# Performance work log

Measured on AMD Instinct MI355X. Metric: run time of the kernel, lower is better.

## Reference

```python
import jax, jax.numpy as jnp
import numpy as np

NUM_SAMPLES = 10
MIN_DIST_PTS = 8
TOP_K = 10
GRID_SIZE = 4
GAP = 0.1


def sample_line_points(seg):
    # seg: [N,2,2] (endpoints, ij coords). Vectorized version of the per-group linspace loop.
    lengths = jnp.linalg.norm(seg[:, 0] - seg[:, 1], axis=1)
    n_samp = jnp.clip(jnp.floor(lengths / MIN_DIST_PTS), 2, NUM_SAMPLES)  # [N]
    t = jnp.arange(NUM_SAMPLES, dtype=seg.dtype)  # [S]
    interval = (seg[:, 1] - seg[:, 0]) / (n_samp[:, None] - 1)  # [N,2]
    pts = seg[:, None, 0, :] + t[None, :, None] * interval[:, None, :]  # [N,S,2]
    valid = t[None, :] < n_samp[:, None]  # [N,S]
    pts = jnp.where(valid[..., None], pts, 0.0)  # original zero-pads invalid samples
    return pts, valid


def grid_sample_norm(desc, pts, img_size):
    # desc: [D,Hc,Wc]; pts: [P,2] (i,j) pixel coords in image of size img_size=(H,W).
    # Replicates kornia normalize_pixel_coordinates + F.grid_sample(align_corners=False,
    # bilinear, zero padding), then L2-normalize along D.
    D, Hc, Wc = desc.shape
    H, W = img_size
    gx = 2.0 * pts[:, 1] / (W - 1) - 1.0
    gy = 2.0 * pts[:, 0] / (H - 1) - 1.0
    ix = ((gx + 1.0) * Wc - 1.0) / 2.0
    iy = ((gy + 1.0) * Hc - 1.0) / 2.0
    x0 = jnp.floor(ix)
    y0 = jnp.floor(iy)
    wx1 = ix - x0
    wy1 = iy - y0
    x0i = x0.astype(jnp.int32)
    y0i = y0.astype(jnp.int32)

    def gather(yi, xi):
        inb = (xi >= 0) & (xi < Wc) & (yi >= 0) & (yi < Hc)
        v = desc[:, jnp.clip(yi, 0, Hc - 1), jnp.clip(xi, 0, Wc - 1)]  # [D,P]
        return v * inb

    v = (gather(y0i, x0i) * (1 - wy1) * (1 - wx1)
         + gather(y0i, x0i + 1) * (1 - wy1) * wx1
         + gather(y0i + 1, x0i) * wy1 * (1 - wx1)
         + gather(y0i + 1, x0i + 1) * wy1 * wx1)
    nrm = jnp.linalg.norm(v, axis=0, keepdims=True)
    return v / jnp.maximum(nrm, 1e-12)


def needleman_wunsch(scores):
    # scores: [B,n,m]. Row-wise scan; the within-row dependency
    # v[j+1]=max(v[j], max(prev[j+1], prev[j]+s)) is a prefix-max (cummax).
    b, n, m = scores.shape
    s = scores - GAP
    init = jnp.zeros((b, m + 1), s.dtype)

    def step(prev, row):  # prev [B,m+1], row [B,m]
        a = jnp.maximum(prev[:, 1:], prev[:, :-1] + row)
        new = jnp.maximum(jax.lax.cummax(a, axis=1), 0.0)
        return jnp.concatenate([jnp.zeros((b, 1), s.dtype), new], axis=1), None

    final, _ = jax.lax.scan(step, init, jnp.swapaxes(s, 0, 1))
    return final[:, -1]


def nw_candidate_scores(scores):
    # scores: [N1,N2,S,S] -> (nw [N1,2k], topk [N1,k])
    ls1 = jnp.max(scores, axis=3)
    v1 = ls1 != -1
    ls1 = jnp.where(v1, ls1, 0.0).sum(2) / v1.sum(2)
    ls2 = jnp.max(scores, axis=2)
    v2 = ls2 != -1
    ls2 = jnp.where(v2, ls2, 0.0).sum(2) / v2.sum(2)
    line_scores = (ls1 + ls2) / 2
    topk = jnp.argsort(line_scores, axis=1)[:, -TOP_K:]  # [N1,k]
    top_scores = jnp.take_along_axis(scores, topk[:, :, None, None], axis=1)  # [N1,k,S,S]
    top_scores = jnp.concatenate([top_scores, jnp.flip(top_scores, axis=-1)], axis=1)  # [N1,2k,S,S]
    N1, t2k, n, m = top_scores.shape
    nw = needleman_wunsch(top_scores.reshape(N1 * t2k, n, m)).reshape(N1, t2k)
    return nw, topk


def filter_and_match(scores):
    nw, topk = nw_candidate_scores(scores)
    t2k = nw.shape[1]
    best = jnp.argmax(nw, axis=1) % (t2k // 2)
    return jnp.take_along_axis(topk, best[:, None], axis=1)[:, 0]


def compute_scores(line_seg1, line_seg2, desc1, desc2):
    S = NUM_SAMPLES
    img1 = (desc1.shape[2] * GRID_SIZE, desc1.shape[3] * GRID_SIZE)
    img2 = (desc2.shape[2] * GRID_SIZE, desc2.shape[3] * GRID_SIZE)
    pts1, val1 = sample_line_points(line_seg1)
    pts2, val2 = sample_line_points(line_seg2)
    d1 = grid_sample_norm(desc1[0], pts1.reshape(-1, 2), img1)  # [D, N1*S]
    d2 = grid_sample_norm(desc2[0], pts2.reshape(-1, 2), img2)  # [D, N2*S]
    sc = d1.T @ d2  # [N1*S, N2*S]
    sc = jnp.where(val1.reshape(-1)[:, None], sc, -1.0)
    sc = jnp.where(val2.reshape(-1)[None, :], sc, -1.0)
    N1, N2 = line_seg1.shape[0], line_seg2.shape[0]
    return sc.reshape(N1, S, N2, S).transpose(0, 2, 1, 3)  # [N1,N2,S,S]


def reference(line_seg1, line_seg2, desc1, desc2):
    scores = compute_scores(line_seg1, line_seg2, desc1, desc2)
    matches = filter_and_match(scores)
    # cross check
    matches2 = filter_and_match(scores.transpose(1, 0, 3, 2))
    mutual = matches2[matches] == jnp.arange(line_seg1.shape[0])
    return jnp.where(mutual, matches, -1).astype(jnp.int32)


def setup_inputs() -> dict:
    key = jax.random.key(0)
    k1, k2, k3, k4 = jax.random.split(key, 4)
    IMG = 512.0
    line_seg1 = jax.random.uniform(k1, (512, 2, 2), dtype=jnp.float32) * (IMG - 1.0)
    line_seg2 = jax.random.uniform(k2, (512, 2, 2), dtype=jnp.float32) * (IMG - 1.0)
    desc1 = jax.random.normal(k3, (1, 128, 128, 128), dtype=jnp.float32)
    desc2 = jax.random.normal(k4, (1, 128, 128, 128), dtype=jnp.float32)
    return {"line_seg1": line_seg1, "line_seg2": line_seg2, "desc1": desc1, "desc2": desc2}
```

## Files before the change

### kernel.cpp

```cpp
#include <hip/hip_runtime.h>
#include <cmath>

#define NL 512
#define SS 10
#define DD 128
#define HWC (128 * 128)

typedef _Float16 f16x8 __attribute__((ext_vector_type(8)));
typedef float f32x4 __attribute__((ext_vector_type(4)));

__device__ __forceinline__ void gload_lds16(const void* g, void* l)
{
    __builtin_amdgcn_global_load_lds(
        (__attribute__((address_space(1))) void*)const_cast<void*>(g),
        (__attribute__((address_space(3))) void*)l, 16, 0, 0);
}

__global__ __launch_bounds__(256) void transpose_kernel(
    const float* __restrict__ in1, const float* __restrict__ in2,
    float* __restrict__ out1, float* __restrict__ out2)
{
    const float* in = blockIdx.z ? in2 : in1;
    float* out = blockIdx.z ? out2 : out1;
    __shared__ float tile[32][33];
    int hw0 = blockIdx.x * 32;
    int d0 = blockIdx.y * 32;
    int tx = threadIdx.x, ty = threadIdx.y;
#pragma unroll
    for (int j = 0; j < 32; j += 8)
        tile[ty + j][tx] = in[(size_t)(d0 + ty + j) * HWC + hw0 + tx];
    __syncthreads();
#pragma unroll
    for (int j = 0; j < 32; j += 8)
        out[(size_t)(hw0 + ty + j) * DD + d0 + tx] = tile[tx][ty + j];
}

__device__ __forceinline__ float fetchd(const float* __restrict__ dt, int y, int x, int d)
{
    bool inb = (x >= 0) && (x < 128) && (y >= 0) && (y < 128);
    int yc = y < 0 ? 0 : (y > 127 ? 127 : y);
    int xc = x < 0 ? 0 : (x > 127 ? 127 : x);
    float v = dt[((size_t)(yc * 128 + xc)) * DD + d];
    return inb ? v : 0.0f;
}

__global__ __launch_bounds__(640) void sample_kernel(
    const float* __restrict__ seg1, const float* __restrict__ seg2,
    const float* __restrict__ dt1, const float* __restrict__ dt2,
    float* __restrict__ dd1, float* __restrict__ dd2,
    _Float16* __restrict__ h1, _Float16* __restrict__ m1,
    _Float16* __restrict__ h2, _Float16* __restrict__ m2,
    int* __restrict__ v1, int* __restrict__ v2)
{
#pragma clang fp contract(off)
    int L = blockIdx.x;
    int img = blockIdx.y;
    const float* seg = img ? seg2 : seg1;
    const float* dt = img ? dt2 : dt1;
    float* dd = img ? dd2 : dd1;
    _Float16* ph = img ? h2 : h1;
    _Float16* pm = img ? m2 : m1;
    int* vv = img ? v2 : v1;

    float p0y = seg[L * 4 + 0], p0x = seg[L * 4 + 1];
    float p1y = seg[L * 4 + 2], p1x = seg[L * 4 + 3];
    float dy = p0y - p1y, dx = p0x - p1x;
    float len = sqrtf(dy * dy + dx * dx);
    float nf = floorf(len / 8.0f);
    nf = fminf(fmaxf(nf, 2.0f), 10.0f);
    int ni = (int)nf;
    float ivy = (p1y - p0y) / (nf - 1.0f);
    float ivx = (p1x - p0x) / (nf - 1.0f);

    int t = threadIdx.x >> 6;
    int lane = threadIdx.x & 63;
    int pt = L * SS + t;
    bool val = t < ni;
    int d0 = lane, d1 = lane + 64;
    float o0 = 0.0f, o1 = 0.0f;
    if (val) {
        float py = p0y + (float)t * ivy;
        float px = p0x + (float)t * ivx;
        float gx = 2.0f * px / 511.0f - 1.0f;
        float gy = 2.0f * py / 511.0f - 1.0f;
        float ix = ((gx + 1.0f) * 128.0f - 1.0f) / 2.0f;
        float iy = ((gy + 1.0f) * 128.0f - 1.0f) / 2.0f;
        float x0f = floorf(ix), y0f = floorf(iy);
        float wx = ix - x0f, wy = iy - y0f;
        int x0 = (int)x0f, y0 = (int)y0f;
        float a00 = fetchd(dt, y0, x0, d0),         b00 = fetchd(dt, y0, x0, d1);
        float a01 = fetchd(dt, y0, x0 + 1, d0),     b01 = fetchd(dt, y0, x0 + 1, d1);
        float a10 = fetchd(dt, y0 + 1, x0, d0),     b10 = fetchd(dt, y0 + 1, x0, d1);
        float a11 = fetchd(dt, y0 + 1, x0 + 1, d0), b11 = fetchd(dt, y0 + 1, x0 + 1, d1);
        float omwx = 1.0f - wx, omwy = 1.0f - wy;
        float va = a00 * omwy * omwx + a01 * omwy * wx + a10 * wy * omwx + a11 * wy * wx;
        float vb = b00 * omwy * omwx + b01 * omwy * wx + b10 * wy * omwx + b11 * wy * wx;
        float s = va * va + vb * vb;
#pragma unroll
        for (int m = 1; m < 64; m <<= 1) s += __shfl_xor(s, m);
        float nrm = sqrtf(s);
        o0 = va / fmaxf(nrm, 1e-12f);
        o1 = vb / fmaxf(nrm, 1e-12f);
    }
    dd[(size_t)pt * DD + d0] = o0;
    dd[(size_t)pt * DD + d1] = o1;
    float xs0 = o0 * 256.0f;
    _Float16 hh0 = (_Float16)xs0;
    _Float16 mm0 = (_Float16)(xs0 - (float)hh0);
    float xs1 = o1 * 256.0f;
    _Float16 hh1 = (_Float16)xs1;
    _Float16 mm1 = (_Float16)(xs1 - (float)hh1);
    int po0 = ((pt >> 4) << 11) + ((d0 >> 3) << 7) + ((pt & 15) << 3) + (d0 & 7);
    int po1 = ((pt >> 4) << 11) + ((d1 >> 3) << 7) + ((pt & 15) << 3) + (d1 & 7);
    ph[po0] = hh0; pm[po0] = mm0;
    ph[po1] = hh1; pm[po1] = mm1;
    if (lane == 0) vv[pt] = val ? 1 : 0;
}

__device__ __forceinline__ void stage_ks(
    const _Float16* __restrict__ ah, const _Float16* __restrict__ am,
    const _Float16* __restrict__ bh, const _Float16* __restrict__ bm,
    int bi, int bj, int ks, int wave, int lane, char* dst)
{
#pragma unroll
    for (int c = 0; c < 8; ++c) {
        int chunk = wave + (c << 3);
        if (chunk < 60) {
            int side = chunk >= 20;
            int rem = side ? chunk - 20 : chunk;
            int nb = side ? 20 : 10;
            int plane = rem >= nb;
            int pb = plane ? rem - nb : rem;
            const _Float16* base = side ? (plane ? bm : bh) : (plane ? am : ah);
            int gpb = side ? (bj * 20 + pb) : (bi * 10 + pb);
            size_t off = ((size_t)gpb << 11) + (ks << 9) + (lane << 3);
            gload_lds16(base + off, dst + (chunk << 10));
        }
    }
}

__global__ __launch_bounds__(512, 2) void gemm_ls_kernel(
    const _Float16* __restrict__ ah_, const _Float16* __restrict__ am_,
    const _Float16* __restrict__ bh_, const _Float16* __restrict__ bm_,
    const int* __restrict__ v1, const int* __restrict__ v2,
    float* __restrict__ ls, float* __restrict__ lsT)
{
    __shared__ __align__(16) char smem[122880];
    int tid = threadIdx.x;
    int wave = tid >> 6, lane = tid & 63;
    int wr = wave >> 2, wc = wave & 3;

    int flat = blockIdx.x;
    int xcd = flat & 7, n = flat >> 3;
    int bi = (xcd >> 1) * 8 + (n >> 3);
    int bj = (xcd & 1) * 8 + (n & 7);

    int fro = ((lane >> 4) << 8) + ((lane & 15) << 4);

    f32x4 zz = {0.0f, 0.0f, 0.0f, 0.0f};
    f32x4 acc[5][5];
#pragma unroll
    for (int i = 0; i < 5; ++i)
#pragma unroll
        for (int j = 0; j < 5; ++j) acc[i][j] = zz;

    stage_ks(ah_, am_, bh_, bm_, bi, bj, 0, wave, lane, smem);

#pragma unroll 1
    for (int ks = 0; ks < 4; ++ks) {
        char* buf = smem + ((ks & 1) ? 61440 : 0);
        if (ks < 3) {
            stage_ks(ah_, am_, bh_, bm_, bi, bj, ks + 1, wave, lane,
                     smem + (((ks + 1) & 1) ? 61440 : 0));
            if (wave < 4) asm volatile("s_waitcnt vmcnt(8)" ::: "memory");
            else          asm volatile("s_waitcnt vmcnt(7)" ::: "memory");
        } else {
            asm volatile("s_waitcnt vmcnt(0)" ::: "memory");
        }
        __builtin_amdgcn_sched_barrier(0);
        __builtin_amdgcn_s_barrier();
        __builtin_amdgcn_sched_barrier(0);

        f16x8 B0[5], B1[5];
#pragma unroll
        for (int j = 0; j < 5; ++j) {
            int pb = wc * 5 + j;
            B0[j] = *(const f16x8*)(buf + ((20 + pb) << 10) + fro);
            B1[j] = *(const f16x8*)(buf + ((40 + pb) << 10) + fro);
        }
#pragma unroll
        for (int i = 0; i < 5; ++i) {
            int pb = wr * 5 + i;
            f16x8 fh = *(const f16x8*)(buf + (pb << 10) + fro);
            f16x8 fm = *(const f16x8*)(buf + ((10 + pb) << 10) + fro);
#pragma unroll
            for (int j = 0; j < 5; ++j) {
                f32x4 t = acc[i][j];
                t = __builtin_amdgcn_mfma_f32_16x16x32_f16(fh, B0[j], t, 0, 0, 0);
                t = __builtin_amdgcn_mfma_f32_16x16x32_f16(fh, B1[j], t, 0, 0, 0);
                t = __builtin_amdgcn_mfma_f32_16x16x32_f16(fm, B0[j], t, 0, 0, 0);
                acc[i][j] = t;
            }
        }
        __builtin_amdgcn_sched_barrier(0);
        __builtin_amdgcn_s_barrier();
        __builtin_amdgcn_sched_barrier(0);
    }

    float* scr = (float*)smem;
    const float rescale = 1.0f / 65536.0f;
    for (int half = 0; half < 2; ++half) {
        __syncthreads();
        if (wr == half) {
            float* reg = scr + wc * 6464;
#pragma unroll
            for (int i = 0; i < 5; ++i)
#pragma unroll
                for (int j = 0; j < 5; ++j)
#pragma unroll
                    for (int r = 0; r < 4; ++r) {
                        int row = i * 16 + ((lane >> 4) << 2) + r;
                        int col = j * 16 + (lane & 15);
                        int pi = row / 10, s = row - pi * 10;
                        int pj = col / 10, t = col - pj * 10;
                        reg[(pi * 8 + pj) * 101 + s * 10 + t] = acc[i][j][r] * rescale;
                    }
            asm volatile("s_waitcnt lgkmcnt(0)" ::: "memory");
            const float* mp = reg + lane * 101;
            int iL = bi * 16 + half * 8 + (lane >> 3);
            int jL = bj * 32 + wc * 8 + (lane & 7);
            int va[10], vb[10];
#pragma unroll
            for (int s = 0; s < 10; ++s) va[s] = v1[iL * 10 + s];
#pragma unroll
            for (int t = 0; t < 10; ++t) vb[t] = v2[jL * 10 + t];
            float cmx[10];
#pragma unroll
            for (int t = 0; t < 10; ++t) cmx[t] = -3.0e38f;
            float sum1 = 0.0f; int c1 = 0;
#pragma unroll
            for (int s = 0; s < 10; ++s) {
                float rmx = -3.0e38f;
#pragma unroll
                for (int t = 0; t < 10; ++t) {
                    float v = (va[s] && vb[t]) ? mp[s * 10 + t] : -1.0f;
                    rmx = fmaxf(rmx, v);
                    cmx[t] = fmaxf(cmx[t], v);
                }
                if (rmx != -1.0f) { sum1 += rmx; c1++; }
            }
            float sum2 = 0.0f; int c2 = 0;
#pragma unroll
            for (int t = 0; t < 10; ++t) {
                if (cmx[t] != -1.0f) { sum2 += cmx[t]; c2++; }
            }
            float out = (sum1 / (float)c1 + sum2 / (float)c2) * 0.5f;
            ls[(size_t)iL * NL + jL] = out;
            lsT[(size_t)jL * NL + iL] = out;
        }
    }
}

__global__ __launch_bounds__(256) void nw_kernel(
    const float* __restrict__ d1, const float* __restrict__ d2,
    const int* __restrict__ v1, const int* __restrict__ v2,
    const float* __restrict__ ls, const float* __restrict__ lsT,
    int* __restrict__ topkg, float* __restrict__ nwout)
{
    int L = blockIdx.x;
    int dir = blockIdx.y;
    const float* Ad = dir ? d2 : d1;
    const float* Bd = dir ? d1 : d2;
    const int* vA = dir ? v2 : v1;
    const int* vB = dir ? v1 : v2;
    const float* src = dir ? &lsT[(size_t)L * NL] : &ls[(size_t)L * NL];

    __shared__ float Asl[10 * 132];
    __shared__ float Bsl[10][1320];
    __shared__ float M[10][110];
    __shared__ int vam[10], tks[10];

    int tid = threadIdx.x;
    if (tid < 10) vam[tid] = vA[L * 10 + tid];
#pragma unroll
    for (int it = 0; it < 5; ++it) {
        int idx = tid + it * 256;
        int row = idx >> 7, col = idx & 127;
        Asl[row * 132 + col] = Ad[((size_t)L * 10 + row) * DD + col];
    }
    if (tid < 64) {
        int lane = tid;
        float v[8];
#pragma unroll
        for (int it = 0; it < 8; ++it) v[it] = src[it * 64 + lane];
        for (int p = 9; p >= 0; --p) {
            float bv = -3.0e38f;
            int bi_ = -1;
#pragma unroll
            for (int it = 0; it < 8; ++it) {
                int j = it * 64 + lane;
                bool better = (v[it] > bv) || (v[it] == bv && j > bi_);
                if (better) { bv = v[it]; bi_ = j; }
            }
#pragma unroll
            for (int m = 1; m < 64; m <<= 1) {
                float ov = __shfl_xor(bv, m);
                int oi = __shfl_xor(bi_, m);
                bool better = (ov > bv) || (ov == bv && oi > bi_);
                if (better) { bv = ov; bi_ = oi; }
            }
            if ((bi_ & 63) == lane) v[bi_ >> 6] = -3.0e38f;
            if (lane == 0) tks[p] = bi_;
        }
    }
    __syncthreads();
    if (tid < 10) topkg[(size_t)(dir * NL + L) * 10 + tid] = tks[tid];
#pragma unroll
    for (int it = 0; it < 50; ++it) {
        int idx = tid + it * 256;
        int c = idx / 1280;
        int rem = idx - c * 1280;
        int row = rem >> 7, col = rem & 127;
        Bsl[c][row * 132 + col] = Bd[((size_t)tks[c] * 10 + row) * DD + col];
    }
    __syncthreads();
#pragma unroll
    for (int it = 0; it < 4; ++it) {
        int w = tid + it * 256;
        if (w < 1000) {
            int c = w / 100;
            int rem = w - c * 100;
            int s = rem / 10, t = rem - s * 10;
            const float4* ap = (const float4*)&Asl[s * 132];
            const float4* bp = (const float4*)&Bsl[c][t * 132];
            float acc = 0.0f;
#pragma unroll
            for (int k = 0; k < 32; ++k) {
                float4 a = ap[k], b = bp[k];
                acc = fmaf(a.x, b.x, acc);
                acc = fmaf(a.y, b.y, acc);
                acc = fmaf(a.z, b.z, acc);
                acc = fmaf(a.w, b.w, acc);
            }
            int ok = vam[s] && vB[tks[c] * 10 + t];
            M[c][s * 11 + t] = ok ? acc : -1.0f;
        }
    }
    __syncthreads();

    if (tid < 20) {
        int c = tid % 10, f = tid / 10;
        float prev[11];
#pragma unroll
        for (int p = 0; p < 11; ++p) prev[p] = 0.0f;
#pragma unroll
        for (int s = 0; s < 10; ++s) {
            float oldp = prev[0];
            float run = -3.0e38f;
#pragma unroll
            for (int t = 0; t < 10; ++t) {
                int tt = f ? (9 - t) : t;
                float sc = M[c][s * 11 + tt] - 0.1f;
                float pt1 = prev[t + 1];
                float av = fmaxf(pt1, oldp + sc);
                run = fmaxf(run, av);
                prev[t + 1] = fmaxf(run, 0.0f);
                oldp = pt1;
            }
        }
        nwout[((size_t)(dir * NL + L)) * 20 + f * 10 + c] = prev[10];
    }
}

__global__ __launch_bounds__(512) void final_kernel(
    const float* __restrict__ nw, const int* __restrict__ topk, int* __restrict__ out)
{
    __shared__ int m1[NL], m2[NL];
    int t = threadIdx.x;
    {
        const float* p = nw + (size_t)t * 20;
        float bb = -3.0e38f; int kk = 0;
        for (int k = 0; k < 20; ++k) {
            float v = p[k];
            if (v > bb) { bb = v; kk = k; }
        }
        m1[t] = topk[(size_t)t * 10 + (kk % 10)];
    }
    {
        const float* p = nw + (size_t)(NL + t) * 20;
        float bb = -3.0e38f; int kk = 0;
        for (int k = 0; k < 20; ++k) {
            float v = p[k];
            if (v > bb) { bb = v; kk = k; }
        }
        m2[t] = topk[(size_t)(NL + t) * 10 + (kk % 10)];
    }
    __syncthreads();
    int mt = m1[t];
    out[t] = (m2[mt] == t) ? mt : -1;
}

extern "C" void kernel_launch(void* const* d_in, const int* in_sizes, int n_in,
                              void* d_out, int out_size, void* d_ws, size_t ws_size,
                              hipStream_t stream)
{
    const float* seg1 = (const float*)d_in[0];
    const float* seg2 = (const float*)d_in[1];
    const float* desc1 = (const float*)d_in[2];
    const float* desc2 = (const float*)d_in[3];
    int* out = (int*)d_out;

    char* ws = (char*)d_ws;
    size_t off = 0;
    float* dt1 = (float*)(ws + off); off += (size_t)DD * HWC * 4;
    float* dt2 = (float*)(ws + off); off += (size_t)DD * HWC * 4;
    float* dd1 = (float*)(ws + off); off += (size_t)NL * SS * DD * 4;
    float* dd2 = (float*)(ws + off); off += (size_t)NL * SS * DD * 4;
    int* v1 = (int*)(ws + off); off += (size_t)NL * SS * 4;
    int* v2 = (int*)(ws + off); off += (size_t)NL * SS * 4;
    float* ls = (float*)(ws + off); off += (size_t)NL * NL * 4;
    float* lsT = (float*)(ws + off); off += (size_t)NL * NL * 4;
    int* topk = (int*)(ws + off); off += (size_t)2 * NL * 10 * 4;
    float* nwv = (float*)(ws + off); off += (size_t)2 * NL * 20 * 4;
    size_t PL = (size_t)NL * SS * DD;
    _Float16* h1 = (_Float16*)(ws + off); off += PL * 2;
    _Float16* m1 = (_Float16*)(ws + off); off += PL * 2;
    _Float16* h2 = (_Float16*)(ws + off); off += PL * 2;
    _Float16* m2 = (_Float16*)(ws + off); off += PL * 2;

    transpose_kernel<<<dim3(HWC / 32, DD / 32, 2), dim3(32, 8), 0, stream>>>(
        desc1, desc2, dt1, dt2);
    sample_kernel<<<dim3(NL, 2), 640, 0, stream>>>(
        seg1, seg2, dt1, dt2, dd1, dd2, h1, m1, h2, m2, v1, v2);
    gemm_ls_kernel<<<512, 512, 0, stream>>>(
        h1, m1, h2, m2, v1, v2, ls, lsT);
    nw_kernel<<<dim3(NL, 2), 256, 0, stream>>>(
        dd1, dd2, v1, v2, ls, lsT, topk, nwv);
    final_kernel<<<1, 512, 0, stream>>>(nwv, topk, out);
}
```

Measured before the change: 182.2 us.

## Replace descriptor transpose with per-channel LDS bilinear sampling plus normalize pass

Removes the full 16MB transpose of both descriptor maps. Each block now loads one 128x128 channel plane into shared memory and bilinearly samples every point from it, writing a channel-major raw buffer. A second kernel transposes tiles of that buffer, L2-normalizes each point and emits the fp32 and hi/lo fp16 split outputs. The aim is to avoid the large transpose read and write traffic, at the cost of an extra intermediate buffer, an extra launch, and a 64KB LDS footprint per block that limits occupancy.

```diff
diff --git a/kernel.cpp b/kernel.cpp
--- a/kernel.cpp
+++ b/kernel.cpp
@@ -5,6 +5,7 @@
 #define SS 10
 #define DD 128
 #define HWC (128 * 128)
+#define NPT (NL * SS)
 
 typedef _Float16 f16x8 __attribute__((ext_vector_type(8)));
 typedef float f32x4 __attribute__((ext_vector_type(4)));
@@ -16,105 +17,135 @@
         (__attribute__((address_space(3))) void*)l, 16, 0, 0);
 }
 
-__global__ __launch_bounds__(256) void transpose_kernel(
-    const float* __restrict__ in1, const float* __restrict__ in2,
-    float* __restrict__ out1, float* __restrict__ out2)
-{
-    const float* in = blockIdx.z ? in2 : in1;
-    float* out = blockIdx.z ? out2 : out1;
-    __shared__ float tile[32][33];
-    int hw0 = blockIdx.x * 32;
-    int d0 = blockIdx.y * 32;
-    int tx = threadIdx.x, ty = threadIdx.y;
-#pragma unroll
-    for (int j = 0; j < 32; j += 8)
-        tile[ty + j][tx] = in[(size_t)(d0 + ty + j) * HWC + hw0 + tx];
-    __syncthreads();
-#pragma unroll
-    for (int j = 0; j < 32; j += 8)
-        out[(size_t)(hw0 + ty + j) * DD + d0 + tx] = tile[tx][ty + j];
-}
-
-__device__ __forceinline__ float fetchd(const float* __restrict__ dt, int y, int x, int d)
-{
-    bool inb = (x >= 0) && (x < 128) && (y >= 0) && (y < 128);
-    int yc = y < 0 ? 0 : (y > 127 ? 127 : y);
-    int xc = x < 0 ? 0 : (x > 127 ? 127 : x);
-    float v = dt[((size_t)(yc * 128 + xc)) * DD + d];
-    return inb ? v : 0.0f;
-}
-
-__global__ __launch_bounds__(640) void sample_kernel(
-    const float* __restrict__ seg1, const float* __restrict__ seg2,
-    const float* __restrict__ dt1, const float* __restrict__ dt2,
-    float* __restrict__ dd1, float* __restrict__ dd2,
-    _Float16* __restrict__ h1, _Float16* __restrict__ m1,
-    _Float16* __restrict__ h2, _Float16* __restrict__ m2,
-    int* __restrict__ v1, int* __restrict__ v2)
+__device__ __forceinline__ void line_geom(const float* __restrict__ seg, int L,
+    float& p0y, float& p0x, float& ivy, float& ivx, int& ni)
 {
 #pragma clang fp contract(off)
-    int L = blockIdx.x;
-    int img = blockIdx.y;
-    const float* seg = img ? seg2 : seg1;
-    const float* dt = img ? dt2 : dt1;
-    float* dd = img ? dd2 : dd1;
-    _Float16* ph = img ? h2 : h1;
-    _Float16* pm = img ? m2 : m1;
-    int* vv = img ? v2 : v1;
-
-    float p0y = seg[L * 4 + 0], p0x = seg[L * 4 + 1];
+    p0y = seg[L * 4 + 0]; p0x = seg[L * 4 + 1];
     float p1y = seg[L * 4 + 2], p1x = seg[L * 4 + 3];
     float dy = p0y - p1y, dx = p0x - p1x;
     float len = sqrtf(dy * dy + dx * dx);
     float nf = floorf(len / 8.0f);
     nf = fminf(fmaxf(nf, 2.0f), 10.0f);
-    int ni = (int)nf;
-    float ivy = (p1y - p0y) / (nf - 1.0f);
-    float ivx = (p1x - p0x) / (nf - 1.0f);
-
-    int t = threadIdx.x >> 6;
-    int lane = threadIdx.x & 63;
-    int pt = L * SS + t;
-    bool val = t < ni;
-    int d0 = lane, d1 = lane + 64;
-    float o0 = 0.0f, o1 = 0.0f;
-    if (val) {
-        float py = p0y + (float)t * ivy;
-        float px = p0x + (float)t * ivx;
-        float gx = 2.0f * px / 511.0f - 1.0f;
-        float gy = 2.0f * py / 511.0f - 1.0f;
-        float ix = ((gx + 1.0f) * 128.0f - 1.0f) / 2.0f;
-        float iy = ((gy + 1.0f) * 128.0f - 1.0f) / 2.0f;
-        float x0f = floorf(ix), y0f = floorf(iy);
-        float wx = ix - x0f, wy = iy - y0f;
-        int x0 = (int)x0f, y0 = (int)y0f;
-        float a00 = fetchd(dt, y0, x0, d0),         b00 = fetchd(dt, y0, x0, d1);
-        float a01 = fetchd(dt, y0, x0 + 1, d0),     b01 = fetchd(dt, y0, x0 + 1, d1);
-        float a10 = fetchd(dt, y0 + 1, x0, d0),     b10 = fetchd(dt, y0 + 1, x0, d1);
-        float a11 = fetchd(dt, y0 + 1, x0 + 1, d0), b11 = fetchd(dt, y0 + 1, x0 + 1, d1);
-        float omwx = 1.0f - wx, omwy = 1.0f - wy;
-        float va = a00 * omwy * omwx + a01 * omwy * wx + a10 * wy * omwx + a11 * wy * wx;
-        float vb = b00 * omwy * omwx + b01 * omwy * wx + b10 * wy * omwx + b11 * wy * wx;
-        float s = va * va + vb * vb;
-#pragma unroll
-        for (int m = 1; m < 64; m <<= 1) s += __shfl_xor(s, m);
-        float nrm = sqrtf(s);
-        o0 = va / fmaxf(nrm, 1e-12f);
-        o1 = vb / fmaxf(nrm, 1e-12f);
-    }
-    dd[(size_t)pt * DD + d0] = o0;
-    dd[(size_t)pt * DD + d1] = o1;
-    float xs0 = o0 * 256.0f;
-    _Float16 hh0 = (_Float16)xs0;
-    _Float16 mm0 = (_Float16)(xs0 - (float)hh0);
-    float xs1 = o1 * 256.0f;
-    _Float16 hh1 = (_Float16)xs1;
-    _Float16 mm1 = (_Float16)(xs1 - (float)hh1);
-    int po0 = ((pt >> 4) << 11) + ((d0 >> 3) << 7) + ((pt & 15) << 3) + (d0 & 7);
-    int po1 = ((pt >> 4) << 11) + ((d1 >> 3) << 7) + ((pt & 15) << 3) + (d1 & 7);
-    ph[po0] = hh0; pm[po0] = mm0;
-    ph[po1] = hh1; pm[po1] = mm1;
-    if (lane == 0) vv[pt] = val ? 1 : 0;
+    ni = (int)nf;
+    ivy = (p1y - p0y) / (nf - 1.0f);
+    ivx = (p1x - p0x) / (nf - 1.0f);
+}
+
+__global__ __launch_bounds__(256) void bilin_kernel(
+    const float* __restrict__ seg1, const float* __restrict__ seg2,
+    const float* __restrict__ desc1, const float* __restrict__ desc2,
+    float* __restrict__ rawT1, float* __restrict__ rawT2)
+{
+#pragma clang fp contract(off)
+    int d = blockIdx.x;
+    int img = blockIdx.y;
+    const float* seg = img ? seg2 : seg1;
+    const float* desc = (img ? desc2 : desc1) + (size_t)d * HWC;
+    float* rawT = (img ? rawT2 : rawT1) + (size_t)d * NPT;
+
+    __shared__ float pd[HWC];
+    int tid = threadIdx.x;
+    const float4* src4 = (const float4*)desc;
+    float4* pd4 = (float4*)pd;
+#pragma unroll
+    for (int i = 0; i < 16; ++i) pd4[tid + i * 256] = src4[tid + i * 256];
+    __syncthreads();
+
+#pragma unroll
+    for (int i = 0; i < 20; ++i) {
+        int pt = tid + i * 256;
+        int L = pt / 10, t = pt - L * 10;
+        float p0y, p0x, ivy, ivx; int ni;
+        line_geom(seg, L, p0y, p0x, ivy, ivx, ni);
+        float outv = 0.0f;
+        if (t < ni) {
+            float py = p0y + (float)t * ivy;
+            float px = p0x + (float)t * ivx;
+            float gx = 2.0f * px / 511.0f - 1.0f;
+            float gy = 2.0f * py / 511.0f - 1.0f;
+            float ix = ((gx + 1.0f) * 128.0f - 1.0f) / 2.0f;
+            float iy = ((gy + 1.0f) * 128.0f - 1.0f) / 2.0f;
+            float x0f = floorf(ix), y0f = floorf(iy);
+            float wx = ix - x0f, wy = iy - y0f;
+            int x0 = (int)x0f, y0 = (int)y0f;
+            int xc0 = x0 < 0 ? 0 : (x0 > 127 ? 127 : x0);
+            int xc1 = (x0 + 1) < 0 ? 0 : ((x0 + 1) > 127 ? 127 : (x0 + 1));
+            int yc0 = y0 < 0 ? 0 : (y0 > 127 ? 127 : y0);
+            int yc1 = (y0 + 1) < 0 ? 0 : ((y0 + 1) > 127 ? 127 : (y0 + 1));
+            bool ibx0 = (x0 >= 0) && (x0 < 128), ibx1 = (x0 + 1 >= 0) && (x0 + 1 < 128);
+            bool iby0 = (y0 >= 0) && (y0 < 128), iby1 = (y0 + 1 >= 0) && (y0 + 1 < 128);
+            float g00 = (ibx0 && iby0) ? pd[yc0 * 128 + xc0] : 0.0f;
+            float g01 = (ibx1 && iby0) ? pd[yc0 * 128 + xc1] : 0.0f;
+            float g10 = (ibx0 && iby1) ? pd[yc1 * 128 + xc0] : 0.0f;
+            float g11 = (ibx1 && iby1) ? pd[yc1 * 128 + xc1] : 0.0f;
+            float omwx = 1.0f - wx, omwy = 1.0f - wy;
+            outv = g00 * omwy * omwx + g01 * omwy * wx + g10 * wy * omwx + g11 * wy * wx;
+        }
+        rawT[pt] = outv;
+    }
+}
+
+__global__ __launch_bounds__(256) void norm_split_kernel(
+    const float* __restrict__ seg1, const float* __restrict__ seg2,
+    const float* __restrict__ rawT1, const float* __restrict__ rawT2,
+    float* __restrict__ dd1, float* __restrict__ dd2,
+    _Float16* __restrict__ h1, _Float16* __restrict__ m1,
+    _Float16* __restrict__ h2, _Float16* __restrict__ m2,
+    int* __restrict__ v1, int* __restrict__ v2)
+{
+#pragma clang fp contract(off)
+    int img = blockIdx.y;
+    int p0 = blockIdx.x * 128;
+    const float* seg = img ? seg2 : seg1;
+    const float* rawT = img ? rawT2 : rawT1;
+    float* dd = img ? dd2 : dd1;
+    _Float16* ph = img ? h2 : h1;
+    _Float16* pm = img ? m2 : m1;
+    int* vv = img ? v2 : v1;
+
+    __shared__ float tile[128][129];
+    __shared__ float nr[128];
+    int tid = threadIdx.x;
+#pragma unroll
+    for (int i = 0; i < 16; ++i) {
+        int idx = tid + i * 256;
+        int r = idx >> 5;
+        int c4 = (idx & 31) << 2;
+        float4 v = *(const float4*)&rawT[(size_t)r * NPT + p0 + c4];
+        tile[r][c4 + 0] = v.x; tile[r][c4 + 1] = v.y;
+        tile[r][c4 + 2] = v.z; tile[r][c4 + 3] = v.w;
+    }
+    __syncthreads();
+    if (tid < 128) {
+        float s = 0.0f;
+#pragma unroll
+        for (int dd_ = 0; dd_ < 128; ++dd_) {
+            float v = tile[dd_][tid];
+            s += v * v;
+        }
+        nr[tid] = fmaxf(sqrtf(s), 1e-12f);
+        int pt = p0 + tid;
+        int L = pt / 10, t = pt - L * 10;
+        float p0y, p0x, ivy, ivx; int ni;
+        line_geom(seg, L, p0y, p0x, ivy, ivx, ni);
+        vv[pt] = (t < ni) ? 1 : 0;
+    }
+    __syncthreads();
+#pragma unroll
+    for (int i = 0; i < 64; ++i) {
+        int idx = tid + i * 256;
+        int ptl = idx >> 7, d = idx & 127;
+        int pt = p0 + ptl;
+        float outv = tile[d][ptl] / nr[ptl];
+        dd[(size_t)pt * DD + d] = outv;
+        float xs = outv * 256.0f;
+        _Float16 hh = (_Float16)xs;
+        _Float16 mm = (_Float16)(xs - (float)hh);
+        int po = ((pt >> 4) << 11) + ((d >> 3) << 7) + ((pt & 15) << 3) + (d & 7);
+        ph[po] = hh;
+        pm[po] = mm;
+    }
 }
 
 __device__ __forceinline__ void stage_ks(
@@ -412,26 +443,26 @@
 
     char* ws = (char*)d_ws;
     size_t off = 0;
-    float* dt1 = (float*)(ws + off); off += (size_t)DD * HWC * 4;
-    float* dt2 = (float*)(ws + off); off += (size_t)DD * HWC * 4;
-    float* dd1 = (float*)(ws + off); off += (size_t)NL * SS * DD * 4;
-    float* dd2 = (float*)(ws + off); off += (size_t)NL * SS * DD * 4;
-    int* v1 = (int*)(ws + off); off += (size_t)NL * SS * 4;
-    int* v2 = (int*)(ws + off); off += (size_t)NL * SS * 4;
+    float* rawT1 = (float*)(ws + off); off += (size_t)NPT * DD * 4;
+    float* rawT2 = (float*)(ws + off); off += (size_t)NPT * DD * 4;
+    float* dd1 = (float*)(ws + off); off += (size_t)NPT * DD * 4;
+    float* dd2 = (float*)(ws + off); off += (size_t)NPT * DD * 4;
+    int* v1 = (int*)(ws + off); off += (size_t)NPT * 4;
+    int* v2 = (int*)(ws + off); off += (size_t)NPT * 4;
     float* ls = (float*)(ws + off); off += (size_t)NL * NL * 4;
     float* lsT = (float*)(ws + off); off += (size_t)NL * NL * 4;
     int* topk = (int*)(ws + off); off += (size_t)2 * NL * 10 * 4;
     float* nwv = (float*)(ws + off); off += (size_t)2 * NL * 20 * 4;
-    size_t PL = (size_t)NL * SS * DD;
+    size_t PL = (size_t)NPT * DD;
     _Float16* h1 = (_Float16*)(ws + off); off += PL * 2;
     _Float16* m1 = (_Float16*)(ws + off); off += PL * 2;
     _Float16* h2 = (_Float16*)(ws + off); off += PL * 2;
     _Float16* m2 = (_Float16*)(ws + off); off += PL * 2;
 
-    transpose_kernel<<<dim3(HWC / 32, DD / 32, 2), dim3(32, 8), 0, stream>>>(
-        desc1, desc2, dt1, dt2);
-    sample_kernel<<<dim3(NL, 2), 640, 0, stream>>>(
-        seg1, seg2, dt1, dt2, dd1, dd2, h1, m1, h2, m2, v1, v2);
+    bilin_kernel<<<dim3(DD, 2), 256, 0, stream>>>(
+        seg1, seg2, desc1, desc2, rawT1, rawT2);
+    norm_split_kernel<<<dim3(NPT / 128, 2), 256, 0, stream>>>(
+        seg1, seg2, rawT1, rawT2, dd1, dd2, h1, m1, h2, m2, v1, v2);
     gemm_ls_kernel<<<512, 512, 0, stream>>>(
         h1, m1, h2, m2, v1, v2, ls, lsT);
     nw_kernel<<<dim3(NL, 2), 256, 0, stream>>>(
```

After: 197.7 us. +8.5%, slower.

## Shrink GEMM tiles with triple-buffered staging and fuse final match into NW kernel

Applied to the files above, without the earlier changes.

The GEMM block tile is halved from 160x320 to 160x160, using 256 threads per block and twice as many blocks. Staging moves from double to triple buffering with two k-steps in flight to hide load latency. The separate final_kernel launch is removed: the last NW block, found through an atomic counter that the transpose kernel resets, does the argmax and the mutual check. This saves a launch and improves GEMM occupancy and balance, but adds atomics and threadfences and keeps 120KB of LDS per block, which may limit residency.

```diff
diff --git a/kernel.cpp b/kernel.cpp
--- a/kernel.cpp
+++ b/kernel.cpp
@@ -18,8 +18,11 @@
 
 __global__ __launch_bounds__(256) void transpose_kernel(
     const float* __restrict__ in1, const float* __restrict__ in2,
-    float* __restrict__ out1, float* __restrict__ out2)
-{
+    float* __restrict__ out1, float* __restrict__ out2, int* __restrict__ cnt)
+{
+    if (blockIdx.x == 0 && blockIdx.y == 0 && blockIdx.z == 0 &&
+        threadIdx.x == 0 && threadIdx.y == 0)
+        atomicExch(cnt, 0);
     const float* in = blockIdx.z ? in2 : in1;
     float* out = blockIdx.z ? out2 : out1;
     __shared__ float tile[32][33];
@@ -123,23 +126,19 @@
     int bi, int bj, int ks, int wave, int lane, char* dst)
 {
 #pragma unroll
-    for (int c = 0; c < 8; ++c) {
-        int chunk = wave + (c << 3);
-        if (chunk < 60) {
-            int side = chunk >= 20;
-            int rem = side ? chunk - 20 : chunk;
-            int nb = side ? 20 : 10;
-            int plane = rem >= nb;
-            int pb = plane ? rem - nb : rem;
-            const _Float16* base = side ? (plane ? bm : bh) : (plane ? am : ah);
-            int gpb = side ? (bj * 20 + pb) : (bi * 10 + pb);
-            size_t off = ((size_t)gpb << 11) + (ks << 9) + (lane << 3);
-            gload_lds16(base + off, dst + (chunk << 10));
-        }
-    }
-}
-
-__global__ __launch_bounds__(512, 2) void gemm_ls_kernel(
+    for (int c = 0; c < 10; ++c) {
+        int chunk = wave * 10 + c;
+        int side = chunk >= 20;
+        int rem = side ? chunk - 20 : chunk;
+        int plane = rem >= 10;
+        int pb = plane ? rem - 10 : rem;
+        const _Float16* base = side ? (plane ? bm : bh) : (plane ? am : ah);
+        size_t off = ((size_t)((side ? bj : bi) * 10 + pb) << 11) + (ks << 9) + (lane << 3);
+        gload_lds16(base + off, dst + (chunk << 10));
+    }
+}
+
+__global__ __launch_bounds__(256, 2) void gemm_ls_kernel(
     const _Float16* __restrict__ ah_, const _Float16* __restrict__ am_,
     const _Float16* __restrict__ bh_, const _Float16* __restrict__ bm_,
     const int* __restrict__ v1, const int* __restrict__ v2,
@@ -148,12 +147,12 @@
     __shared__ __align__(16) char smem[122880];
     int tid = threadIdx.x;
     int wave = tid >> 6, lane = tid & 63;
-    int wr = wave >> 2, wc = wave & 3;
+    int wr = wave >> 1, wc = wave & 1;
 
     int flat = blockIdx.x;
     int xcd = flat & 7, n = flat >> 3;
-    int bi = (xcd >> 1) * 8 + (n >> 3);
-    int bj = (xcd & 1) * 8 + (n & 7);
+    int bi = (xcd >> 1) * 8 + (n >> 4);
+    int bj = (xcd & 1) * 16 + (n & 15);
 
     int fro = ((lane >> 4) << 8) + ((lane & 15) << 4);
 
@@ -165,15 +164,17 @@
         for (int j = 0; j < 5; ++j) acc[i][j] = zz;
 
     stage_ks(ah_, am_, bh_, bm_, bi, bj, 0, wave, lane, smem);
+    stage_ks(ah_, am_, bh_, bm_, bi, bj, 1, wave, lane, smem + 40960);
 
 #pragma unroll 1
     for (int ks = 0; ks < 4; ++ks) {
-        char* buf = smem + ((ks & 1) ? 61440 : 0);
-        if (ks < 3) {
-            stage_ks(ah_, am_, bh_, bm_, bi, bj, ks + 1, wave, lane,
-                     smem + (((ks + 1) & 1) ? 61440 : 0));
-            if (wave < 4) asm volatile("s_waitcnt vmcnt(8)" ::: "memory");
-            else          asm volatile("s_waitcnt vmcnt(7)" ::: "memory");
+        char* buf = smem + 40960 * (ks % 3);
+        if (ks < 2) {
+            stage_ks(ah_, am_, bh_, bm_, bi, bj, ks + 2, wave, lane,
+                     smem + 40960 * ((ks + 2) % 3));
+            asm volatile("s_waitcnt vmcnt(20)" ::: "memory");
+        } else if (ks == 2) {
+            asm volatile("s_waitcnt vmcnt(10)" ::: "memory");
         } else {
             asm volatile("s_waitcnt vmcnt(0)" ::: "memory");
         }
@@ -186,7 +187,7 @@
         for (int j = 0; j < 5; ++j) {
             int pb = wc * 5 + j;
             B0[j] = *(const f16x8*)(buf + ((20 + pb) << 10) + fro);
-            B1[j] = *(const f16x8*)(buf + ((40 + pb) << 10) + fro);
+            B1[j] = *(const f16x8*)(buf + ((30 + pb) << 10) + fro);
         }
 #pragma unroll
         for (int i = 0; i < 5; ++i) {
@@ -228,7 +229,7 @@
             asm volatile("s_waitcnt lgkmcnt(0)" ::: "memory");
             const float* mp = reg + lane * 101;
             int iL = bi * 16 + half * 8 + (lane >> 3);
-            int jL = bj * 32 + wc * 8 + (lane & 7);
+            int jL = bj * 16 + wc * 8 + (lane & 7);
             int va[10], vb[10];
 #pragma unroll
             for (int s = 0; s < 10; ++s) va[s] = v1[iL * 10 + s];
@@ -265,7 +266,8 @@
     const float* __restrict__ d1, const float* __restrict__ d2,
     const int* __restrict__ v1, const int* __restrict__ v2,
     const float* __restrict__ ls, const float* __restrict__ lsT,
-    int* __restrict__ topkg, float* __restrict__ nwout)
+    int* __restrict__ topkg, float* __restrict__ nwout,
+    int* __restrict__ cnt, int* __restrict__ outg)
 {
     int L = blockIdx.x;
     int dir = blockIdx.y;
@@ -279,6 +281,8 @@
     __shared__ float Bsl[10][1320];
     __shared__ float M[10][110];
     __shared__ int vam[10], tks[10];
+    __shared__ int lastflag;
+    __shared__ int m1f[NL], m2f[NL];
 
     int tid = threadIdx.x;
     if (tid < 10) vam[tid] = vA[L * 10 + tid];
@@ -370,34 +374,44 @@
         }
         nwout[((size_t)(dir * NL + L)) * 20 + f * 10 + c] = prev[10];
     }
-}
-
-__global__ __launch_bounds__(512) void final_kernel(
-    const float* __restrict__ nw, const int* __restrict__ topk, int* __restrict__ out)
-{
-    __shared__ int m1[NL], m2[NL];
-    int t = threadIdx.x;
-    {
-        const float* p = nw + (size_t)t * 20;
-        float bb = -3.0e38f; int kk = 0;
-        for (int k = 0; k < 20; ++k) {
-            float v = p[k];
-            if (v > bb) { bb = v; kk = k; }
-        }
-        m1[t] = topk[(size_t)t * 10 + (kk % 10)];
-    }
-    {
-        const float* p = nw + (size_t)(NL + t) * 20;
-        float bb = -3.0e38f; int kk = 0;
-        for (int k = 0; k < 20; ++k) {
-            float v = p[k];
-            if (v > bb) { bb = v; kk = k; }
-        }
-        m2[t] = topk[(size_t)(NL + t) * 10 + (kk % 10)];
-    }
-    __syncthreads();
-    int mt = m1[t];
-    out[t] = (m2[mt] == t) ? mt : -1;
+    __syncthreads();
+    if (tid == 0) {
+        __threadfence();
+        lastflag = (atomicAdd(cnt, 1) == 2 * NL - 1) ? 1 : 0;
+    }
+    __syncthreads();
+    if (!lastflag) return;
+
+    __threadfence();
+#pragma unroll
+    for (int rep = 0; rep < 2; ++rep) {
+        int t = tid + rep * 256;
+        {
+            const float* p = nwout + (size_t)t * 20;
+            float bb = -3.0e38f; int kk = 0;
+            for (int k = 0; k < 20; ++k) {
+                float v = p[k];
+                if (v > bb) { bb = v; kk = k; }
+            }
+            m1f[t] = topkg[(size_t)t * 10 + (kk % 10)];
+        }
+        {
+            const float* p = nwout + (size_t)(NL + t) * 20;
+            float bb = -3.0e38f; int kk = 0;
+            for (int k = 0; k < 20; ++k) {
+                float v = p[k];
+                if (v > bb) { bb = v; kk = k; }
+            }
+            m2f[t] = topkg[(size_t)(NL + t) * 10 + (kk % 10)];
+        }
+    }
+    __syncthreads();
+#pragma unroll
+    for (int rep = 0; rep < 2; ++rep) {
+        int t = tid + rep * 256;
+        int mt = m1f[t];
+        outg[t] = (m2f[mt] == t) ? mt : -1;
+    }
 }
 
 extern "C" void kernel_launch(void* const* d_in, const int* in_sizes, int n_in,
@@ -422,6 +436,7 @@
     float* lsT = (float*)(ws + off); off += (size_t)NL * NL * 4;
     int* topk = (int*)(ws + off); off += (size_t)2 * NL * 10 * 4;
     float* nwv = (float*)(ws + off); off += (size_t)2 * NL * 20 * 4;
+    int* cnt = (int*)(ws + off); off += 256;
     size_t PL = (size_t)NL * SS * DD;
     _Float16* h1 = (_Float16*)(ws + off); off += PL * 2;
     _Float16* m1 = (_Float16*)(ws + off); off += PL * 2;
@@ -429,12 +444,11 @@
     _Float16* m2 = (_Float16*)(ws + off); off += PL * 2;
 
     transpose_kernel<<<dim3(HWC / 32, DD / 32, 2), dim3(32, 8), 0, stream>>>(
-        desc1, desc2, dt1, dt2);
+        desc1, desc2, dt1, dt2, cnt);
     sample_kernel<<<dim3(NL, 2), 640, 0, stream>>>(
         seg1, seg2, dt1, dt2, dd1, dd2, h1, m1, h2, m2, v1, v2);
-    gemm_ls_kernel<<<512, 512, 0, stream>>>(
+    gemm_ls_kernel<<<1024, 256, 0, stream>>>(
         h1, m1, h2, m2, v1, v2, ls, lsT);
     nw_kernel<<<dim3(NL, 2), 256, 0, stream>>>(
-        dd1, dd2, v1, v2, ls, lsT, topk, nwv);
-    final_kernel<<<1, 512, 0, stream>>>(nwv, topk, out);
-}
+        dd1, dd2, v1, v2, ls, lsT, topk, nwv, cnt, out);
+}
```

Result: faster. 174.5 us (-4.2%).
